# Kernel tuning notes

Hardware: AMD Instinct MI355X
Metric: run time of the kernel (lower is better)

Reference implementation:

```python
import jax, jax.numpy as jnp
import numpy as np

N = 4096    # channels * n = 4 * 1024
N_IN = 1024
FC = 512


def ldr_layer(x, G, H, subd_A, subd_B, bias):
    """y = W x + bias, where W = sum_i K(A, g_i) K(B, h_i)^T and A, B are
    subdiagonal matrices with entries subd_A, subd_B (Krylov LDR fast multiply).

    Closed form: K(A, g)[i, j] = g[i-j] * c[i] / c[i-j] for i >= j (0 otherwise),
    with c = [1, cumprod(subd_A)]. This turns the multiply into FFT
    correlations/convolutions of length 2n instead of a dense n x n GEMM.
    x: (b, n); G, H: (r, n); subd_A, subd_B: (n-1,); bias: (n,).
    """
    n = x.shape[-1]
    one = jnp.ones((1,), x.dtype)
    c = jnp.concatenate([one, jnp.cumprod(subd_A)])   # (n,) cumulative subdiag products of A
    d = jnp.concatenate([one, jnp.cumprod(subd_B)])   # (n,)
    L = 2 * n
    q = H / d                                          # (r, n)
    gp = G / c                                         # (r, n)
    p = x * d                                          # (b, n)
    # u[b, r, j] = (K(B, h_r)^T x)[j] = sum_k q[r, k] * p[b, j + k]  (cross-correlation)
    Fp = jnp.fft.rfft(p, n=L)                          # (b, n+1)
    Fq = jnp.fft.rfft(q, n=L)                          # (r, n+1)
    u = jnp.fft.irfft(Fp[:, None] * jnp.conj(Fq)[None], n=L)[..., :n]  # (b, r, n)
    # out[b, i] = c[i] * sum_r (gp_r * u[b, r])_conv[i]  (causal convolution)
    Fg = jnp.fft.rfft(gp, n=L)                         # (r, n+1)
    Fu = jnp.fft.rfft(u, n=L)                          # (b, r, n+1)
    out = jnp.fft.irfft(jnp.einsum('rk,brk->bk', Fg, Fu), n=L)[:, :n]
    return c * out + bias


def setup_inputs() -> dict:
    key = jax.random.key(0)
    ks = jax.random.split(key, 14)
    std = 0.01  # params.init_stddev
    f32 = jnp.float32
    inp = {
        'x': jax.random.normal(ks[0], (128, N_IN), f32),
        'G1': std * jax.random.normal(ks[1], (48, N), f32),
        'H1': std * jax.random.normal(ks[2], (48, N), f32),
        'subd_A1': jnp.exp(0.01 * jax.random.normal(ks[3], (N - 1,), f32)),
        'subd_B1': jnp.exp(0.01 * jax.random.normal(ks[4], (N - 1,), f32)),
        'b1': std * jax.random.normal(ks[5], (N,), f32),
        'G2': std * jax.random.normal(ks[6], (16, N), f32),
        'H2': std * jax.random.normal(ks[7], (16, N), f32),
        'subd_A2': jnp.exp(0.01 * jax.random.normal(ks[8], (N - 1,), f32)),
        'subd_B2': jnp.exp(0.01 * jax.random.normal(ks[9], (N - 1,), f32)),
        'b2': std * jax.random.normal(ks[10], (N,), f32),
        'W_logits': jax.random.normal(ks[11], (10, FC), f32) / np.sqrt(FC).astype(np.float32),
        'b_logits': std * jax.random.normal(ks[12], (10,), f32),
    }
    return inp


def reference(x, G1, H1, subd_A1, subd_B1, b1, G2, H2, subd_A2, subd_B2, b2,
              W_logits, b_logits):
    bsz, n_in = x.shape
    xp = jnp.concatenate([x, jnp.zeros((bsz, N - n_in), x.dtype)], axis=-1)  # pad to channels*n
    h = jax.nn.relu(ldr_layer(xp, G1, H1, subd_A1, subd_B1, b1))
    h = jax.nn.relu(ldr_layer(h, G2, H2, subd_A2, subd_B2, b2))
    return h[:, :FC] @ W_logits.T + b_logits
```

## Files before the change

### kernel.cpp

```cpp
#include <hip/hip_runtime.h>
#include <hip/hip_bf16.h>

#define BATCH 128
#define NIN   1024
#define NFULL 4096
#define R1    48
#define R2    16
#define FCDIM 512
#define NOUT  10

#define WS_C1  0
#define WS_D1  4096
#define WS_C2  8192
#define WS_D2  12288
#define WS_Q1  16384
#define WS_GP1 (WS_Q1 + R1*NFULL)
#define WS_Q2  (WS_GP1 + R1*NFULL)
#define WS_GP2 (WS_Q2 + R2*NFULL)
#define WS_P1  (WS_GP2 + R2*NFULL)
#define WS_P2  (WS_P1 + BATCH*NIN)
#define WS_H2  (WS_P2 + BATCH*NFULL)
#define WS_PT1 (WS_H2 + BATCH*FCDIM)
#define WS_P2M (WS_PT1 + NIN*NFULL)
#define WS_CT1 (WS_P2M + FCDIM*NFULL)
#define WS_CT2 (WS_CT1 + 16*5120)
#define WS_VP1 (WS_CT2 + 8*4608)
#define WS_VP2 (WS_VP1 + 4*BATCH*NFULL)
#define WS_END (WS_VP2 + 32*BATCH*FCDIM)

#define NCH1 16
#define NCH2 8
#define CHROWS 64
#define CTLD1 5120
#define CTLD2 4608

__global__ void __launch_bounds__(256) prep_fused(
    const float* __restrict__ x, const float* __restrict__ G1,
    const float* __restrict__ H1, const float* __restrict__ G2,
    const float* __restrict__ H2, const float* __restrict__ sA1,
    const float* __restrict__ sB1, const float* __restrict__ sA2,
    const float* __restrict__ sB2, float* __restrict__ ws) {
    __shared__ float cd[4096];
    __shared__ float tot[256];
    int b = blockIdx.x, t = threadIdx.x;
    const float* src;
    int kind, r;
    if (b < 48)       { kind = 0; r = b;       src = sB1; }
    else if (b < 96)  { kind = 1; r = b - 48;  src = sA1; }
    else if (b < 112) { kind = 2; r = b - 96;  src = sB2; }
    else if (b < 128) { kind = 3; r = b - 112; src = sA2; }
    else              { kind = 4; r = b - 128; src = sB1; }
    float loc[16];
    float prod = 1.f;
#pragma unroll
    for (int u = 0; u < 16; ++u) {
        int idx = t * 16 + u;
        float e = (idx == 0) ? 1.f : src[idx - 1];
        prod *= e;
        loc[u] = prod;
    }
    tot[t] = prod;
    __syncthreads();
    for (int off = 1; off < 256; off <<= 1) {
        float v = (t >= off) ? tot[t - off] : 1.f;
        __syncthreads();
        tot[t] *= v;
        __syncthreads();
    }
    float excl = (t == 0) ? 1.f : tot[t - 1];
#pragma unroll
    for (int u = 0; u < 16; ++u) cd[t * 16 + u] = excl * loc[u];
    __syncthreads();

    if (kind == 0) {
        const float* s0 = H1 + (size_t)r * NFULL;
        float* dst = ws + WS_Q1 + (size_t)r * NFULL;
#pragma unroll
        for (int u = 0; u < 16; ++u) { int i = t + u * 256; dst[i] = s0[i] / cd[i]; }
        if (r == 0) { float* d1 = ws + WS_D1;
#pragma unroll
            for (int u = 0; u < 16; ++u) { int i = t + u * 256; d1[i] = cd[i]; } }
    } else if (kind == 1) {
        const float* s0 = G1 + (size_t)r * NFULL;
        float* dst = ws + WS_GP1 + (size_t)r * NFULL;
#pragma unroll
        for (int u = 0; u < 16; ++u) { int i = t + u * 256; dst[i] = s0[i] / cd[i]; }
        if (r == 0) { float* c1 = ws + WS_C1;
#pragma unroll
            for (int u = 0; u < 16; ++u) { int i = t + u * 256; c1[i] = cd[i]; } }
    } else if (kind == 2) {
        const float* s0 = H2 + (size_t)r * NFULL;
        float* dst = ws + WS_Q2 + (size_t)r * NFULL;
#pragma unroll
        for (int u = 0; u < 16; ++u) { int i = t + u * 256; dst[i] = s0[i] / cd[i]; }
        if (r == 0) { float* d2 = ws + WS_D2;
#pragma unroll
            for (int u = 0; u < 16; ++u) { int i = t + u * 256; d2[i] = cd[i]; } }
    } else if (kind == 3) {
        const float* s0 = G2 + (size_t)r * NFULL;
        float* dst = ws + WS_GP2 + (size_t)r * NFULL;
#pragma unroll
        for (int u = 0; u < 16; ++u) { int i = t + u * 256; dst[i] = s0[i] / cd[i]; }
        if (r == 0) { float* c2 = ws + WS_C2;
#pragma unroll
            for (int u = 0; u < 16; ++u) { int i = t + u * 256; c2[i] = cd[i]; } }
    } else {
        int row0 = r * 4;
#pragma unroll
        for (int u = 0; u < 16; ++u) {
            int lin = t + u * 256;
            int row = row0 + (lin >> 10), col = lin & 1023;
            ws[WS_P1 + (size_t)row * NIN + col] = x[(size_t)row * NIN + col] * cd[col];
        }
    }
}

__global__ void __launch_bounds__(256) gemm_rank_kernel(float* __restrict__ ws) {
    const int which = blockIdx.z;
    if (which == 1 && blockIdx.y >= 8) return;
    const float* A = ws + (which == 0 ? WS_Q1  : WS_GP2);
    const float* B = ws + (which == 0 ? WS_GP1 : WS_Q2);
    float* C       = ws + (which == 0 ? WS_PT1 : WS_P2M);
    const int Kr   = which == 0 ? R1 : R2;
    __shared__ float As[R1 * 68];
    __shared__ float Bs[R1 * 68];
    int tid = threadIdx.x;
    int tx = tid & 15, ty = tid >> 4;
    int n0 = blockIdx.x * 64;
    int m0 = blockIdx.y * 64;
    int nf4 = Kr * 16;
    for (int lin = tid; lin < nf4; lin += 256) {
        int r = lin >> 4, i4 = lin & 15;
        *(float4*)&As[r * 68 + i4 * 4] = *(const float4*)&A[(size_t)r * NFULL + m0 + i4 * 4];
        *(float4*)&Bs[r * 68 + i4 * 4] = *(const float4*)&B[(size_t)r * NFULL + n0 + i4 * 4];
    }
    __syncthreads();
    float acc[4][4] = {};
#pragma unroll 8
    for (int r = 0; r < Kr; ++r) {
        float4 a4 = *(const float4*)&As[r * 68 + ty * 4];
        float4 b4 = *(const float4*)&Bs[r * 68 + tx * 4];
        acc[0][0] += a4.x * b4.x; acc[0][1] += a4.x * b4.y;
        acc[0][2] += a4.x * b4.z; acc[0][3] += a4.x * b4.w;
        acc[1][0] += a4.y * b4.x; acc[1][1] += a4.y * b4.y;
        acc[1][2] += a4.y * b4.z; acc[1][3] += a4.y * b4.w;
        acc[2][0] += a4.z * b4.x; acc[2][1] += a4.z * b4.y;
        acc[2][2] += a4.z * b4.z; acc[2][3] += a4.z * b4.w;
        acc[3][0] += a4.w * b4.x; acc[3][1] += a4.w * b4.y;
        acc[3][2] += a4.w * b4.z; acc[3][3] += a4.w * b4.w;
    }
#pragma unroll
    for (int i = 0; i < 4; ++i) {
        int m = m0 + ty * 4 + i;
        *(float4*)&C[(size_t)m * NFULL + n0 + tx * 4] =
            make_float4(acc[i][0], acc[i][1], acc[i][2], acc[i][3]);
    }
}

__global__ void diag_scan_p1(float* __restrict__ ws) {
    const int which = blockIdx.z;
    const int nch   = which == 0 ? NCH1 : NCH2;
    if (blockIdx.y >= (unsigned)nch) return;
    float* P        = ws + (which == 0 ? WS_PT1 : WS_P2M);
    float* ctot     = ws + (which == 0 ? WS_CT1 : WS_CT2);
    const int R     = which == 0 ? NIN : FCDIM;
    const int nd    = R + NFULL - 1;
    const int ctld  = which == 0 ? CTLD1 : CTLD2;
    int t = blockIdx.x * 256 + threadIdx.x;
    if (t >= nd) return;
    int doff = t - (R - 1);
    int z = blockIdx.y;
    int m0 = z * CHROWS;
    int mlo = max(m0, -doff);
    int mhi = min(m0 + CHROWS, min(NFULL - doff, R));
    float run = 0.f;
    if (mlo < mhi) {
        float* p = P + (size_t)mlo * NFULL + (mlo + doff);
        const size_t step = NFULL + 1;
        int len = mhi - mlo;
        int s = 0;
        for (; s + 16 <= len; s += 16) {
            float v[16];
#pragma unroll
            for (int u = 0; u < 16; ++u) v[u] = p[u * step];
#pragma unroll
            for (int u = 0; u < 16; ++u) { run += v[u]; v[u] = run; }
#pragma unroll
            for (int u = 0; u < 16; ++u) p[u * step] = v[u];
            p += 16 * step;
        }
        for (; s < len; ++s) { float v = *p; run += v; *p = run; p += step; }
    }
    ctot[(size_t)z * ctld + t] = run;
}

__global__ void off_prefix(float* __restrict__ ws) {
    const int which = blockIdx.z;
    float* ct      = ws + (which == 0 ? WS_CT1 : WS_CT2);
    const int ctld = which == 0 ? CTLD1 : CTLD2;
    const int nch  = which == 0 ? NCH1 : NCH2;
    int t = blockIdx.x * 256 + threadIdx.x;
    if (t >= ctld) return;
    float run = 0.f;
    for (int z = 0; z < nch; ++z) {
        float v = ct[(size_t)z * ctld + t];
        ct[(size_t)z * ctld + t] = run;
        run += v;
    }
}

__global__ void __launch_bounds__(1024)
gemm2_l1_kernel(const float* __restrict__ p1, const float* __restrict__ Mt1,
                const float* __restrict__ OFF1, float* __restrict__ vp) {
    __shared__ float As[2][32][132];
    __shared__ float Bs[2][32][68];
    int tid = threadIdx.x;
    int g = tid >> 9;
    int t = tid & 511;
    int tx = t & 15, ty = t >> 4;
    int n0 = blockIdx.x * 64;
    int kbase = blockIdx.z * 256 + g * 128;
    float acc[4][4] = {};
    for (int k0 = kbase; k0 < kbase + 128; k0 += 32) {
        const float* orow = OFF1 + (size_t)(k0 >> 6) * CTLD1;
#pragma unroll
        for (int l = 0; l < 2; ++l) {
            int lin = t + l * 512;
            int m = lin >> 3, k4 = lin & 7;
            float4 v = *(const float4*)&p1[(size_t)m * NIN + k0 + k4 * 4];
            As[g][k4 * 4 + 0][m] = v.x;
            As[g][k4 * 4 + 1][m] = v.y;
            As[g][k4 * 4 + 2][m] = v.z;
            As[g][k4 * 4 + 3][m] = v.w;
        }
        {
            int k = t >> 4, n4 = t & 15;
            float4 v = *(const float4*)&Mt1[(size_t)(k0 + k) * NFULL + n0 + n4 * 4];
            const float* o = &orow[1023 + n0 + n4 * 4 - (k0 + k)];
            v.x += o[0]; v.y += o[1]; v.z += o[2]; v.w += o[3];
            *(float4*)&Bs[g][k][n4 * 4] = v;
        }
        __syncthreads();
#pragma unroll
        for (int kk = 0; kk < 32; ++kk) {
            float4 a4 = *(const float4*)&As[g][kk][ty * 4];
            float4 b4 = *(const float4*)&Bs[g][kk][tx * 4];
            acc[0][0] += a4.x * b4.x; acc[0][1] += a4.x * b4.y;
            acc[0][2] += a4.x * b4.z; acc[0][3] += a4.x * b4.w;
            acc[1][0] += a4.y * b4.x; acc[1][1] += a4.y * b4.y;
            acc[1][2] += a4.y * b4.z; acc[1][3] += a4.y * b4.w;
            acc[2][0] += a4.z * b4.x; acc[2][1] += a4.z * b4.y;
            acc[2][2] += a4.z * b4.z; acc[2][3] += a4.z * b4.w;
            acc[3][0] += a4.w * b4.x; acc[3][1] += a4.w * b4.y;
            acc[3][2] += a4.w * b4.z; acc[3][3] += a4.w * b4.w;
        }
        __syncthreads();
    }
    float* red = &As[0][0][0];
    if (g == 1) {
#pragma unroll
        for (int i = 0; i < 4; ++i)
            *(float4*)&red[(ty * 4 + i) * 64 + tx * 4] =
                make_float4(acc[i][0], acc[i][1], acc[i][2], acc[i][3]);
    }
    __syncthreads();
    if (g == 0) {
        float* dst = vp + (size_t)blockIdx.z * BATCH * NFULL;
#pragma unroll
        for (int i = 0; i < 4; ++i) {
            int m = ty * 4 + i;
            float4 r = *(const float4*)&red[m * 64 + tx * 4];
            *(float4*)&dst[(size_t)m * NFULL + n0 + tx * 4] =
                make_float4(acc[i][0] + r.x, acc[i][1] + r.y,
                            acc[i][2] + r.z, acc[i][3] + r.w);
        }
    }
}

__global__ void reduce_l1_kernel(const float* __restrict__ vp, const float* __restrict__ c1,
                                 const float* __restrict__ b1, const float* __restrict__ d2,
                                 float* __restrict__ p2) {
    int idx4 = blockIdx.x * 256 + threadIdx.x;
    int base = idx4 * 4;
    int n = base & (NFULL - 1);
    float4 s = make_float4(0.f, 0.f, 0.f, 0.f);
#pragma unroll
    for (int z = 0; z < 4; ++z) {
        float4 v = *(const float4*)&vp[(size_t)z * BATCH * NFULL + base];
        s.x += v.x; s.y += v.y; s.z += v.z; s.w += v.w;
    }
    float4 cc = *(const float4*)&c1[n];
    float4 bb = *(const float4*)&b1[n];
    float4 dd = *(const float4*)&d2[n];
    float4 o;
    o.x = fmaxf(cc.x * s.x + bb.x, 0.f) * dd.x;
    o.y = fmaxf(cc.y * s.y + bb.y, 0.f) * dd.y;
    o.z = fmaxf(cc.z * s.z + bb.z, 0.f) * dd.z;
    o.w = fmaxf(cc.w * s.w + bb.w, 0.f) * dd.w;
    *(float4*)&p2[base] = o;
}

__global__ void __launch_bounds__(512)
gemm2_l2_kernel(const float* __restrict__ p2, const float* __restrict__ M2,
                const float* __restrict__ OFF2, float* __restrict__ vp) {
    __shared__ float As[32][132];
    __shared__ float Bs[32][68];
    int t = threadIdx.x;
    int tx = t & 15, ty = t >> 4;
    int n0 = blockIdx.x * 64;
    int kbase = blockIdx.z * 128;
    const float* offrow = OFF2 + (size_t)(n0 >> 6) * CTLD2;
    float acc[4][4] = {};
    for (int k0 = kbase; k0 < kbase + 128; k0 += 32) {
#pragma unroll
        for (int l = 0; l < 2; ++l) {
            int lin = t + l * 512;
            int m = lin >> 3, k4 = lin & 7;
            float4 v = *(const float4*)&p2[(size_t)m * NFULL + k0 + k4 * 4];
            As[k4 * 4 + 0][m] = v.x;
            As[k4 * 4 + 1][m] = v.y;
            As[k4 * 4 + 2][m] = v.z;
            As[k4 * 4 + 3][m] = v.w;
        }
        {
            int n = t >> 3, k4 = t & 7;
            float4 v = *(const float4*)&M2[(size_t)(n0 + n) * NFULL + k0 + k4 * 4];
            const float* o = &offrow[511 + k0 + k4 * 4 - (n0 + n)];
            v.x += o[0]; v.y += o[1]; v.z += o[2]; v.w += o[3];
            Bs[k4 * 4 + 0][n] = v.x;
            Bs[k4 * 4 + 1][n] = v.y;
            Bs[k4 * 4 + 2][n] = v.z;
            Bs[k4 * 4 + 3][n] = v.w;
        }
        __syncthreads();
#pragma unroll
        for (int kk = 0; kk < 32; ++kk) {
            float4 a4 = *(const float4*)&As[kk][ty * 4];
            float4 b4 = *(const float4*)&Bs[kk][tx * 4];
            acc[0][0] += a4.x * b4.x; acc[0][1] += a4.x * b4.y;
            acc[0][2] += a4.x * b4.z; acc[0][3] += a4.x * b4.w;
            acc[1][0] += a4.y * b4.x; acc[1][1] += a4.y * b4.y;
            acc[1][2] += a4.y * b4.z; acc[1][3] += a4.y * b4.w;
            acc[2][0] += a4.z * b4.x; acc[2][1] += a4.z * b4.y;
            acc[2][2] += a4.z * b4.z; acc[2][3] += a4.z * b4.w;
            acc[3][0] += a4.w * b4.x; acc[3][1] += a4.w * b4.y;
            acc[3][2] += a4.w * b4.z; acc[3][3] += a4.w * b4.w;
        }
        __syncthreads();
    }
#pragma unroll
    for (int i = 0; i < 4; ++i) {
        int m = ty * 4 + i;
        *(float4*)&vp[((size_t)blockIdx.z * BATCH + m) * FCDIM + n0 + tx * 4] =
            make_float4(acc[i][0], acc[i][1], acc[i][2], acc[i][3]);
    }
}

__global__ void fused_out_kernel(const float* __restrict__ vp, const float* __restrict__ c2,
                                 const float* __restrict__ b2, const float* __restrict__ Wl,
                                 const float* __restrict__ bl, float* __restrict__ out) {
    __shared__ float h2s[FCDIM];
    int b = blockIdx.x, t = threadIdx.x;
    for (int col = t; col < FCDIM; col += 256) {
        float s = 0.f;
#pragma unroll
        for (int z = 0; z < 32; ++z)
            s += vp[((size_t)z * BATCH + b) * FCDIM + col];
        h2s[col] = fmaxf(c2[col] * s + b2[col], 0.f);
    }
    __syncthreads();
    int w = t >> 6, lane = t & 63;
    for (int o = w; o < NOUT; o += 4) {
        float s = 0.f;
#pragma unroll
        for (int i = lane; i < FCDIM; i += 64) s += h2s[i] * Wl[(size_t)o * FCDIM + i];
#pragma unroll
        for (int off = 32; off > 0; off >>= 1) s += __shfl_down(s, off);
        if (lane == 0) out[(size_t)b * NOUT + o] = s + bl[o];
    }
}

extern "C" void kernel_launch(void* const* d_in, const int* in_sizes, int n_in,
                              void* d_out, int out_size, void* d_ws, size_t ws_size,
                              hipStream_t stream) {
    const float* x   = (const float*)d_in[0];
    const float* G1  = (const float*)d_in[1];
    const float* H1  = (const float*)d_in[2];
    const float* sA1 = (const float*)d_in[3];
    const float* sB1 = (const float*)d_in[4];
    const float* b1  = (const float*)d_in[5];
    const float* G2  = (const float*)d_in[6];
    const float* H2  = (const float*)d_in[7];
    const float* sA2 = (const float*)d_in[8];
    const float* sB2 = (const float*)d_in[9];
    const float* b2  = (const float*)d_in[10];
    const float* Wl  = (const float*)d_in[11];
    const float* bl  = (const float*)d_in[12];
    float* out = (float*)d_out;
    float* ws = (float*)d_ws;
    (void)in_sizes; (void)n_in; (void)out_size; (void)ws_size;

    prep_fused<<<160, 256, 0, stream>>>(x, G1, H1, G2, H2, sA1, sB1, sA2, sB2, ws);

    gemm_rank_kernel<<<dim3(64, 16, 2), 256, 0, stream>>>(ws);

    diag_scan_p1<<<dim3(20, NCH1, 2), 256, 0, stream>>>(ws);
    off_prefix<<<dim3(20, 1, 2), 256, 0, stream>>>(ws);

    gemm2_l1_kernel<<<dim3(64, 1, 4), 1024, 0, stream>>>(ws + WS_P1, ws + WS_PT1,
                                                         ws + WS_CT1, ws + WS_VP1);
    reduce_l1_kernel<<<512, 256, 0, stream>>>(ws + WS_VP1, ws + WS_C1, b1, ws + WS_D2,
                                              ws + WS_P2);

    gemm2_l2_kernel<<<dim3(8, 1, 32), 512, 0, stream>>>(ws + WS_P2, ws + WS_P2M,
                                                        ws + WS_CT2, ws + WS_VP2);

    fused_out_kernel<<<BATCH, 256, 0, stream>>>(ws + WS_VP2, ws + WS_C2, b2, Wl, bl, out);
}
```

Before: 79.89 us.

## Replace FP32 SIMT GEMMs with split-bf16 MFMA GEMMs for both layers

Both large GEMMs move from FP32 FMA loops to bf16 MFMA 16x16x32 instructions. Each operand is split into a high and a low bf16 part, and three products (hh, hl, lh) are summed to keep accuracy close to FP32. Activations are stored pre-split as bf16 pairs by the prep and reduce kernels. The weight-side operand is split on the fly, either through a software-pipelined LDS stage (layer 1) or directly in registers (layer 2). The aim is to use matrix cores instead of vector ALUs, at the cost of 3x MFMA work and extra conversion arithmetic, with a small precision risk.

```diff
diff --git a/kernel.cpp b/kernel.cpp
--- a/kernel.cpp
+++ b/kernel.cpp
@@ -34,6 +34,19 @@
 #define CTLD1 5120
 #define CTLD2 4608
 
+typedef __attribute__((ext_vector_type(8))) short bf16x8;
+typedef __attribute__((ext_vector_type(4))) float f32x4;
+
+__device__ __forceinline__ unsigned short f2b(float f) {
+    unsigned u = __builtin_bit_cast(unsigned, f);
+    return (unsigned short)((u + 0x7fffu + ((u >> 16) & 1u)) >> 16);
+}
+__device__ __forceinline__ float b2f(unsigned short h) {
+    unsigned u = ((unsigned)h) << 16;
+    return __builtin_bit_cast(float, u);
+}
+#define MFMA16(a, b, c) __builtin_amdgcn_mfma_f32_16x16x32_bf16(a, b, c, 0, 0, 0)
+
 __global__ void __launch_bounds__(256) prep_fused(
     const float* __restrict__ x, const float* __restrict__ G1,
     const float* __restrict__ H1, const float* __restrict__ G2,
@@ -105,12 +118,17 @@
 #pragma unroll
             for (int u = 0; u < 16; ++u) { int i = t + u * 256; c2[i] = cd[i]; } }
     } else {
+        unsigned short* p1h = (unsigned short*)(ws + WS_P1);
+        unsigned short* p1l = p1h + BATCH * NIN;
         int row0 = r * 4;
 #pragma unroll
         for (int u = 0; u < 16; ++u) {
             int lin = t + u * 256;
             int row = row0 + (lin >> 10), col = lin & 1023;
-            ws[WS_P1 + (size_t)row * NIN + col] = x[(size_t)row * NIN + col] * cd[col];
+            float f = x[(size_t)row * NIN + col] * cd[col];
+            unsigned short h = f2b(f);
+            p1h[(size_t)row * NIN + col] = h;
+            p1l[(size_t)row * NIN + col] = f2b(f - b2f(h));
         }
     }
 }
@@ -209,77 +227,96 @@
     }
 }
 
-__global__ void __launch_bounds__(1024)
-gemm2_l1_kernel(const float* __restrict__ p1, const float* __restrict__ Mt1,
-                const float* __restrict__ OFF1, float* __restrict__ vp) {
-    __shared__ float As[2][32][132];
-    __shared__ float Bs[2][32][68];
-    int tid = threadIdx.x;
-    int g = tid >> 9;
-    int t = tid & 511;
-    int tx = t & 15, ty = t >> 4;
-    int n0 = blockIdx.x * 64;
-    int kbase = blockIdx.z * 256 + g * 128;
-    float acc[4][4] = {};
-    for (int k0 = kbase; k0 < kbase + 128; k0 += 32) {
-        const float* orow = OFF1 + (size_t)(k0 >> 6) * CTLD1;
-#pragma unroll
-        for (int l = 0; l < 2; ++l) {
-            int lin = t + l * 512;
-            int m = lin >> 3, k4 = lin & 7;
-            float4 v = *(const float4*)&p1[(size_t)m * NIN + k0 + k4 * 4];
-            As[g][k4 * 4 + 0][m] = v.x;
-            As[g][k4 * 4 + 1][m] = v.y;
-            As[g][k4 * 4 + 2][m] = v.z;
-            As[g][k4 * 4 + 3][m] = v.w;
-        }
-        {
-            int k = t >> 4, n4 = t & 15;
-            float4 v = *(const float4*)&Mt1[(size_t)(k0 + k) * NFULL + n0 + n4 * 4];
-            const float* o = &orow[1023 + n0 + n4 * 4 - (k0 + k)];
-            v.x += o[0]; v.y += o[1]; v.z += o[2]; v.w += o[3];
-            *(float4*)&Bs[g][k][n4 * 4] = v;
-        }
-        __syncthreads();
-#pragma unroll
-        for (int kk = 0; kk < 32; ++kk) {
-            float4 a4 = *(const float4*)&As[g][kk][ty * 4];
-            float4 b4 = *(const float4*)&Bs[g][kk][tx * 4];
-            acc[0][0] += a4.x * b4.x; acc[0][1] += a4.x * b4.y;
-            acc[0][2] += a4.x * b4.z; acc[0][3] += a4.x * b4.w;
-            acc[1][0] += a4.y * b4.x; acc[1][1] += a4.y * b4.y;
-            acc[1][2] += a4.y * b4.z; acc[1][3] += a4.y * b4.w;
-            acc[2][0] += a4.z * b4.x; acc[2][1] += a4.z * b4.y;
-            acc[2][2] += a4.z * b4.z; acc[2][3] += a4.z * b4.w;
-            acc[3][0] += a4.w * b4.x; acc[3][1] += a4.w * b4.y;
-            acc[3][2] += a4.w * b4.z; acc[3][3] += a4.w * b4.w;
-        }
-        __syncthreads();
-    }
-    float* red = &As[0][0][0];
-    if (g == 1) {
-#pragma unroll
-        for (int i = 0; i < 4; ++i)
-            *(float4*)&red[(ty * 4 + i) * 64 + tx * 4] =
-                make_float4(acc[i][0], acc[i][1], acc[i][2], acc[i][3]);
-    }
-    __syncthreads();
-    if (g == 0) {
-        float* dst = vp + (size_t)blockIdx.z * BATCH * NFULL;
-#pragma unroll
-        for (int i = 0; i < 4; ++i) {
-            int m = ty * 4 + i;
-            float4 r = *(const float4*)&red[m * 64 + tx * 4];
-            *(float4*)&dst[(size_t)m * NFULL + n0 + tx * 4] =
-                make_float4(acc[i][0] + r.x, acc[i][1] + r.y,
-                            acc[i][2] + r.z, acc[i][3] + r.w);
-        }
+#define L1_LOADA(H0, H1, L0, L1v, KS) { \
+    int kk_ = kbase + (KS) * 32 + 8 * g; \
+    const unsigned short* pa_ = p1h + (size_t)(mq * 32 + lm) * NIN + kk_; \
+    const unsigned short* pb_ = p1l + (size_t)(mq * 32 + lm) * NIN + kk_; \
+    H0 = *(const bf16x8*)pa_;  H1 = *(const bf16x8*)(pa_ + 16 * NIN); \
+    L0 = *(const bf16x8*)pb_;  L1v = *(const bf16x8*)(pb_ + 16 * NIN); }
+
+#define L1_LOADS(KS) { \
+    int kg_ = kbase + (KS) * 32 + 2 * k2; \
+    const float* pr_ = P1 + (size_t)kg_ * NFULL + n0 + 2 * n2; \
+    float2 va_ = *(const float2*)pr_; \
+    float2 vb_ = *(const float2*)(pr_ + NFULL); \
+    const float* orow_ = OFF1 + (size_t)(kg_ >> 6) * CTLD1 + (1023 + n0 + 2 * n2 - kg_); \
+    float om_ = orow_[-1], oc_ = orow_[0], op_ = orow_[1]; \
+    f00 = va_.x + oc_; f01 = va_.y + op_; f10 = vb_.x + om_; f11 = vb_.y + oc_; }
+
+#define L1_WRITES() { \
+    unsigned short h00_ = f2b(f00), h10_ = f2b(f10), h01_ = f2b(f01), h11_ = f2b(f11); \
+    int a0_ = (2 * n2) * 20 + k2; \
+    Bh[a0_]      = (unsigned)h00_ | ((unsigned)h10_ << 16); \
+    Bh[a0_ + 20] = (unsigned)h01_ | ((unsigned)h11_ << 16); \
+    Bl[a0_]      = (unsigned)f2b(f00 - b2f(h00_)) | ((unsigned)f2b(f10 - b2f(h10_)) << 16); \
+    Bl[a0_ + 20] = (unsigned)f2b(f01 - b2f(h01_)) | ((unsigned)f2b(f11 - b2f(h11_)) << 16); }
+
+#define L1_COMPUTE(H0, H1, L0, L1v) { \
+    int nb_ = (nh * 32 + lm) * 20 + 4 * g; \
+    uint4 uh0_ = *(const uint4*)&Bh[nb_];       uint4 ul0_ = *(const uint4*)&Bl[nb_]; \
+    uint4 uh1_ = *(const uint4*)&Bh[nb_ + 320]; uint4 ul1_ = *(const uint4*)&Bl[nb_ + 320]; \
+    bf16x8 bh0_ = __builtin_bit_cast(bf16x8, uh0_), bl0_ = __builtin_bit_cast(bf16x8, ul0_); \
+    bf16x8 bh1_ = __builtin_bit_cast(bf16x8, uh1_), bl1_ = __builtin_bit_cast(bf16x8, ul1_); \
+    acc00 = MFMA16(H0, bh0_, acc00); acc10 = MFMA16(H1, bh0_, acc10); \
+    acc01 = MFMA16(H0, bh1_, acc01); acc11 = MFMA16(H1, bh1_, acc11); \
+    acc00 = MFMA16(H0, bl0_, acc00); acc10 = MFMA16(H1, bl0_, acc10); \
+    acc01 = MFMA16(H0, bl1_, acc01); acc11 = MFMA16(H1, bl1_, acc11); \
+    acc00 = MFMA16(L0, bh0_, acc00); acc10 = MFMA16(L1v, bh0_, acc10); \
+    acc01 = MFMA16(L0, bh1_, acc01); acc11 = MFMA16(L1v, bh1_, acc11); }
+
+#define L1_STEP(CH0, CH1, CL0, CL1, NH0, NH1, NL0, NL1, KS, LAST) \
+    __syncthreads(); \
+    L1_WRITES(); \
+    if (!(LAST)) { L1_LOADS((KS) + 1); L1_LOADA(NH0, NH1, NL0, NL1, (KS) + 1); } \
+    __syncthreads(); \
+    L1_COMPUTE(CH0, CH1, CL0, CL1);
+
+__global__ void __launch_bounds__(512)
+gemm2_l1_mfma(const float* __restrict__ P1, const float* __restrict__ OFF1,
+              const unsigned short* __restrict__ p1h,
+              const unsigned short* __restrict__ p1l, float* __restrict__ vp) {
+    __shared__ unsigned Bh[64 * 20];
+    __shared__ unsigned Bl[64 * 20];
+    const int t = threadIdx.x;
+    const int n0 = blockIdx.x * 64;
+    const int kbase = blockIdx.z * 256;
+    const int w = t >> 6, l = t & 63;
+    const int mq = w >> 1, nh = w & 1;
+    const int lm = l & 15, g = l >> 4;
+    const int k2 = t >> 5, n2 = t & 31;
+
+    f32x4 zero = {0.f, 0.f, 0.f, 0.f};
+    f32x4 acc00 = zero, acc01 = zero, acc10 = zero, acc11 = zero;
+    bf16x8 ahA0, ahA1, alA0, alA1, ahB0, ahB1, alB0, alB1;
+    float f00, f01, f10, f11;
+
+    L1_LOADS(0);
+    L1_LOADA(ahA0, ahA1, alA0, alA1, 0);
+    L1_STEP(ahA0, ahA1, alA0, alA1, ahB0, ahB1, alB0, alB1, 0, 0)
+    L1_STEP(ahB0, ahB1, alB0, alB1, ahA0, ahA1, alA0, alA1, 1, 0)
+    L1_STEP(ahA0, ahA1, alA0, alA1, ahB0, ahB1, alB0, alB1, 2, 0)
+    L1_STEP(ahB0, ahB1, alB0, alB1, ahA0, ahA1, alA0, alA1, 3, 0)
+    L1_STEP(ahA0, ahA1, alA0, alA1, ahB0, ahB1, alB0, alB1, 4, 0)
+    L1_STEP(ahB0, ahB1, alB0, alB1, ahA0, ahA1, alA0, alA1, 5, 0)
+    L1_STEP(ahA0, ahA1, alA0, alA1, ahB0, ahB1, alB0, alB1, 6, 0)
+    L1_STEP(ahB0, ahB1, alB0, alB1, ahA0, ahA1, alA0, alA1, 7, 1)
+
+    float* dst = vp + (size_t)blockIdx.z * BATCH * NFULL;
+    int row0 = mq * 32 + 4 * g;
+    int col0 = n0 + nh * 32 + lm;
+#pragma unroll
+    for (int r = 0; r < 4; ++r) {
+        dst[(size_t)(row0 + r) * NFULL + col0]           = acc00[r];
+        dst[(size_t)(row0 + r) * NFULL + col0 + 16]      = acc01[r];
+        dst[(size_t)(row0 + 16 + r) * NFULL + col0]      = acc10[r];
+        dst[(size_t)(row0 + 16 + r) * NFULL + col0 + 16] = acc11[r];
     }
 }
 
 __global__ void reduce_l1_kernel(const float* __restrict__ vp, const float* __restrict__ c1,
                                  const float* __restrict__ b1, const float* __restrict__ d2,
-                                 float* __restrict__ p2) {
+                                 unsigned short* __restrict__ p2h,
+                                 unsigned short* __restrict__ p2l) {
     int idx4 = blockIdx.x * 256 + threadIdx.x;
     int base = idx4 * 4;
     int n = base & (NFULL - 1);
@@ -292,67 +329,80 @@
     float4 cc = *(const float4*)&c1[n];
     float4 bb = *(const float4*)&b1[n];
     float4 dd = *(const float4*)&d2[n];
-    float4 o;
-    o.x = fmaxf(cc.x * s.x + bb.x, 0.f) * dd.x;
-    o.y = fmaxf(cc.y * s.y + bb.y, 0.f) * dd.y;
-    o.z = fmaxf(cc.z * s.z + bb.z, 0.f) * dd.z;
-    o.w = fmaxf(cc.w * s.w + bb.w, 0.f) * dd.w;
-    *(float4*)&p2[base] = o;
+    float f[4];
+    f[0] = fmaxf(cc.x * s.x + bb.x, 0.f) * dd.x;
+    f[1] = fmaxf(cc.y * s.y + bb.y, 0.f) * dd.y;
+    f[2] = fmaxf(cc.z * s.z + bb.z, 0.f) * dd.z;
+    f[3] = fmaxf(cc.w * s.w + bb.w, 0.f) * dd.w;
+    ushort4 hv, lv;
+    unsigned short h;
+    h = f2b(f[0]); hv.x = h; lv.x = f2b(f[0] - b2f(h));
+    h = f2b(f[1]); hv.y = h; lv.y = f2b(f[1] - b2f(h));
+    h = f2b(f[2]); hv.z = h; lv.z = f2b(f[2] - b2f(h));
+    h = f2b(f[3]); hv.w = h; lv.w = f2b(f[3] - b2f(h));
+    *(ushort4*)&p2h[base] = hv;
+    *(ushort4*)&p2l[base] = lv;
 }
 
 __global__ void __launch_bounds__(512)
-gemm2_l2_kernel(const float* __restrict__ p2, const float* __restrict__ M2,
-                const float* __restrict__ OFF2, float* __restrict__ vp) {
-    __shared__ float As[32][132];
-    __shared__ float Bs[32][68];
-    int t = threadIdx.x;
-    int tx = t & 15, ty = t >> 4;
-    int n0 = blockIdx.x * 64;
-    int kbase = blockIdx.z * 128;
-    const float* offrow = OFF2 + (size_t)(n0 >> 6) * CTLD2;
-    float acc[4][4] = {};
-    for (int k0 = kbase; k0 < kbase + 128; k0 += 32) {
-#pragma unroll
-        for (int l = 0; l < 2; ++l) {
-            int lin = t + l * 512;
-            int m = lin >> 3, k4 = lin & 7;
-            float4 v = *(const float4*)&p2[(size_t)m * NFULL + k0 + k4 * 4];
-            As[k4 * 4 + 0][m] = v.x;
-            As[k4 * 4 + 1][m] = v.y;
-            As[k4 * 4 + 2][m] = v.z;
-            As[k4 * 4 + 3][m] = v.w;
+gemm2_l2_mfma(const unsigned short* __restrict__ p2h,
+              const unsigned short* __restrict__ p2l,
+              const float* __restrict__ M2, const float* __restrict__ OFF2,
+              float* __restrict__ vp) {
+    const int t = threadIdx.x;
+    const int n0 = blockIdx.x * 64;
+    const int kbase = blockIdx.z * 128;
+    const int w = t >> 6, l = t & 63;
+    const int mq = w >> 1, nh = w & 1;
+    const int lm = l & 15, g = l >> 4;
+    f32x4 zero = {0.f, 0.f, 0.f, 0.f};
+    f32x4 acc00 = zero, acc01 = zero, acc10 = zero, acc11 = zero;
+    const int nn0 = n0 + nh * 32 + lm;
+    const int nn1 = nn0 + 16;
+    const float* om0 = OFF2 + (size_t)(nn0 >> 6) * CTLD2 + (511 - nn0);
+    const float* om1 = OFF2 + (size_t)(nn1 >> 6) * CTLD2 + (511 - nn1);
+#pragma unroll
+    for (int ks = 0; ks < 4; ++ks) {
+        int kk = kbase + ks * 32 + 8 * g;
+        const unsigned short* pa = p2h + (size_t)(mq * 32 + lm) * NFULL + kk;
+        const unsigned short* pb = p2l + (size_t)(mq * 32 + lm) * NFULL + kk;
+        bf16x8 ah0 = *(const bf16x8*)pa, ah1 = *(const bf16x8*)(pa + 16 * NFULL);
+        bf16x8 al0 = *(const bf16x8*)pb, al1 = *(const bf16x8*)(pb + 16 * NFULL);
+        bf16x8 bh0, bl0, bh1, bl1;
+        {
+            const float* pm = M2 + (size_t)nn0 * NFULL + kk;
+#pragma unroll
+            for (int r = 0; r < 8; ++r) {
+                float f = pm[r] + om0[kk + r];
+                unsigned short h = f2b(f);
+                bh0[r] = (short)h; bl0[r] = (short)f2b(f - b2f(h));
+            }
         }
         {
-            int n = t >> 3, k4 = t & 7;
-            float4 v = *(const float4*)&M2[(size_t)(n0 + n) * NFULL + k0 + k4 * 4];
-            const float* o = &offrow[511 + k0 + k4 * 4 - (n0 + n)];
-            v.x += o[0]; v.y += o[1]; v.z += o[2]; v.w += o[3];
-            Bs[k4 * 4 + 0][n] = v.x;
-            Bs[k4 * 4 + 1][n] = v.y;
-            Bs[k4 * 4 + 2][n] = v.z;
-            Bs[k4 * 4 + 3][n] = v.w;
+            const float* pm = M2 + (size_t)nn1 * NFULL + kk;
+#pragma unroll
+            for (int r = 0; r < 8; ++r) {
+                float f = pm[r] + om1[kk + r];
+                unsigned short h = f2b(f);
+                bh1[r] = (short)h; bl1[r] = (short)f2b(f - b2f(h));
+            }
         }
-        __syncthreads();
-#pragma unroll
-        for (int kk = 0; kk < 32; ++kk) {
-            float4 a4 = *(const float4*)&As[kk][ty * 4];
-            float4 b4 = *(const float4*)&Bs[kk][tx * 4];
-            acc[0][0] += a4.x * b4.x; acc[0][1] += a4.x * b4.y;
-            acc[0][2] += a4.x * b4.z; acc[0][3] += a4.x * b4.w;
-            acc[1][0] += a4.y * b4.x; acc[1][1] += a4.y * b4.y;
-            acc[1][2] += a4.y * b4.z; acc[1][3] += a4.y * b4.w;
-            acc[2][0] += a4.z * b4.x; acc[2][1] += a4.z * b4.y;
-            acc[2][2] += a4.z * b4.z; acc[2][3] += a4.z * b4.w;
-            acc[3][0] += a4.w * b4.x; acc[3][1] += a4.w * b4.y;
-            acc[3][2] += a4.w * b4.z; acc[3][3] += a4.w * b4.w;
-        }
-        __syncthreads();
-    }
-#pragma unroll
-    for (int i = 0; i < 4; ++i) {
-        int m = ty * 4 + i;
-        *(float4*)&vp[((size_t)blockIdx.z * BATCH + m) * FCDIM + n0 + tx * 4] =
-            make_float4(acc[i][0], acc[i][1], acc[i][2], acc[i][3]);
+        acc00 = MFMA16(ah0, bh0, acc00); acc10 = MFMA16(ah1, bh0, acc10);
+        acc01 = MFMA16(ah0, bh1, acc01); acc11 = MFMA16(ah1, bh1, acc11);
+        acc00 = MFMA16(ah0, bl0, acc00); acc10 = MFMA16(ah1, bl0, acc10);
+        acc01 = MFMA16(ah0, bl1, acc01); acc11 = MFMA16(ah1, bl1, acc11);
+        acc00 = MFMA16(al0, bh0, acc00); acc10 = MFMA16(al1, bh0, acc10);
+        acc01 = MFMA16(al0, bh1, acc01); acc11 = MFMA16(al1, bh1, acc11);
+    }
+    float* dst = vp + (size_t)blockIdx.z * BATCH * FCDIM;
+    int row0 = mq * 32 + 4 * g;
+    int col0 = n0 + nh * 32 + lm;
+#pragma unroll
+    for (int r = 0; r < 4; ++r) {
+        dst[(size_t)(row0 + r) * FCDIM + col0]           = acc00[r];
+        dst[(size_t)(row0 + r) * FCDIM + col0 + 16]      = acc01[r];
+        dst[(size_t)(row0 + 16 + r) * FCDIM + col0]      = acc10[r];
+        dst[(size_t)(row0 + 16 + r) * FCDIM + col0 + 16] = acc11[r];
     }
 }
 
@@ -400,6 +450,11 @@
     float* ws = (float*)d_ws;
     (void)in_sizes; (void)n_in; (void)out_size; (void)ws_size;
 
+    unsigned short* p1h = (unsigned short*)(ws + WS_P1);
+    unsigned short* p1l = p1h + BATCH * NIN;
+    unsigned short* p2h = (unsigned short*)(ws + WS_P2);
+    unsigned short* p2l = p2h + BATCH * NFULL;
+
     prep_fused<<<160, 256, 0, stream>>>(x, G1, H1, G2, H2, sA1, sB1, sA2, sB2, ws);
 
     gemm_rank_kernel<<<dim3(64, 16, 2), 256, 0, stream>>>(ws);
@@ -407,13 +462,13 @@
     diag_scan_p1<<<dim3(20, NCH1, 2), 256, 0, stream>>>(ws);
     off_prefix<<<dim3(20, 1, 2), 256, 0, stream>>>(ws);
 
-    gemm2_l1_kernel<<<dim3(64, 1, 4), 1024, 0, stream>>>(ws + WS_P1, ws + WS_PT1,
-                                                         ws + WS_CT1, ws + WS_VP1);
+    gemm2_l1_mfma<<<dim3(64, 1, 4), 512, 0, stream>>>(ws + WS_PT1, ws + WS_CT1,
+                                                      p1h, p1l, ws + WS_VP1);
     reduce_l1_kernel<<<512, 256, 0, stream>>>(ws + WS_VP1, ws + WS_C1, b1, ws + WS_D2,
-                                              ws + WS_P2);
-
-    gemm2_l2_kernel<<<dim3(8, 1, 32), 512, 0, stream>>>(ws + WS_P2, ws + WS_P2M,
-                                                        ws + WS_CT2, ws + WS_VP2);
+                                              p2h, p2l);
+
+    gemm2_l2_mfma<<<dim3(8, 1, 32), 512, 0, stream>>>(p2h, p2l, ws + WS_P2M,
+                                                      ws + WS_CT2, ws + WS_VP2);
 
     fused_out_kernel<<<BATCH, 256, 0, stream>>>(ws + WS_VP2, ws + WS_C2, b2, Wl, bl, out);
 }
```

New measurement: 70.94 us (median of 2 runs). 1.13x faster.
